# Performance work log

Measured on AMD Instinct MI355X. Metric: run time of the kernel, lower is better.

Reference implementation:

```python
import jax, jax.numpy as jnp
import numpy as np
import math

NUM_BUCKETS = 32
MAX_DISTANCE = 128
N_HEAD = 16
HEAD_DIM = 64
HIDDEN = 1024


def _rel_buckets(S):
    """T5 bidirectional relative-position buckets, [q, k] int32."""
    half = NUM_BUCKETS // 2            # 16
    max_exact = half // 2              # 8
    coeff = (half - max_exact) / math.log(MAX_DISTANCE / max_exact)
    pos = jnp.arange(S, dtype=jnp.int32)
    rel = pos[None, :] - pos[:, None]  # mem_pos - ctx_pos, shape [q, k]
    arel = jnp.abs(rel)
    base = jnp.where(rel > 0, half, 0)
    # log-spaced buckets for distant positions (trunc toward zero == floor here since arg >= 0)
    distant = max_exact + (
        jnp.log(jnp.maximum(arel, 1).astype(jnp.float32) / max_exact) * coeff
    ).astype(jnp.int32)
    distant = jnp.minimum(distant, half - 1)
    return base + jnp.where(arel < max_exact, arel, distant)


def setup_inputs() -> dict:
    key = jax.random.key(0)
    k1, k2, k3, k4 = jax.random.split(key, 4)
    B, S = 2, 2048
    std = 1.0 / math.sqrt(HIDDEN)
    x = jax.random.normal(k1, (B, S, HIDDEN), dtype=jnp.float32)
    emb_weight = jax.random.normal(k2, (NUM_BUCKETS, N_HEAD), dtype=jnp.float32) * 0.5
    qkv_w = jax.random.normal(k3, (3 * N_HEAD * HEAD_DIM, HIDDEN), dtype=jnp.float32) * std
    o_w = jax.random.normal(k4, (HIDDEN, N_HEAD * HEAD_DIM), dtype=jnp.float32) * std
    return {"x": x, "emb_weight": emb_weight, "qkv_w": qkv_w, "o_w": o_w}


def reference(x, emb_weight, qkv_w, o_w):
    B, S, D = x.shape
    qkv = x @ qkv_w.T                                   # [B, S, 3*H*hd]
    qkv = qkv.reshape(B, S, 3, N_HEAD, HEAD_DIM)
    q = qkv[:, :, 0].transpose(0, 2, 1, 3)              # [B, H, S, hd]
    k = qkv[:, :, 1].transpose(0, 2, 1, 3)
    v = qkv[:, :, 2].transpose(0, 2, 1, 3)
    bias = emb_weight[_rel_buckets(S)]                  # [q, k, H]
    bias = bias.transpose(2, 0, 1)[None]                # [1, H, q, k]
    scale = HEAD_DIM ** -0.5
    scores = jnp.einsum('bhqd,bhkd->bhqk', q, k) * scale + bias
    attn = jax.nn.softmax(scores, axis=-1)
    a = jnp.einsum('bhqk,bhkd->bhqd', attn, v)          # [B, H, S, hd]
    a = a.transpose(0, 2, 1, 3).reshape(B, S, N_HEAD * HEAD_DIM)
    return a @ o_w.T
```

## Files before the change

### kernel.cpp

```cpp
#include <hip/hip_runtime.h>

#define S_LEN 2048
#define NH 16
#define HD 64
#define DMODEL 1024

typedef __attribute__((ext_vector_type(8))) short bf16x8;
typedef __attribute__((ext_vector_type(4))) float f32x4;

__device__ inline unsigned short f2bf(float f) {
  union { float f; unsigned u; } v; v.f = f;
  unsigned r = v.u + 0x7FFFu + ((v.u >> 16) & 1u);
  return (unsigned short)(r >> 16);
}

__device__ inline void async16(void* lds, const void* g) {
  __builtin_amdgcn_global_load_lds((__attribute__((address_space(1))) void*)(g),
                                   (__attribute__((address_space(3))) void*)(lds),
                                   16, 0, 0);
}

__global__ __launch_bounds__(256) void prep_kernel(
    const float* __restrict__ x, const float* __restrict__ emb,
    const float* __restrict__ qkv_w, const float* __restrict__ o_w,
    unsigned short* __restrict__ xb, unsigned short* __restrict__ wb,
    unsigned short* __restrict__ ob, float* __restrict__ biasg) {
  if (blockIdx.x >= 8192) {
    int h = blockIdx.x - 8192;
    for (int i = threadIdx.x; i < 4095; i += 256) {
      int rel = i - 2047;
      int a = rel < 0 ? -rel : rel;
      int bucket;
      if (a < 8) bucket = a;
      else bucket = 8 + (a >= 12) + (a >= 16) + (a >= 23) + (a >= 32) +
                        (a >= 46) + (a >= 64) + (a >= 91);
      if (rel > 0) bucket += 16;
      biasg[h * 4096 + i] = emb[bucket * NH + h] * 1.4426950408889634f;
    }
    return;
  }
  const int NX = 2 * S_LEN * DMODEL / 4;
  const int NW = 3 * NH * HD * DMODEL / 4;
  int j = blockIdx.x * 256 + threadIdx.x;
  const float* s; unsigned short* d;
  if (j < NX)            { s = x;     d = xb; }
  else if (j < NX + NW)  { j -= NX;      s = qkv_w; d = wb; }
  else                   { j -= NX + NW; s = o_w;   d = ob; }
  float4 v = ((const float4*)s)[j];
  ushort4 p;
  p.x = f2bf(v.x); p.y = f2bf(v.y); p.z = f2bf(v.z); p.w = f2bf(v.w);
  ((ushort4*)d)[j] = p;
}

__global__ __launch_bounds__(256) void qkv_gemm_kernel(
    const unsigned short* __restrict__ xb, const unsigned short* __restrict__ wb,
    unsigned short* __restrict__ Qg, unsigned short* __restrict__ Kg,
    unsigned short* __restrict__ Vtg) {
  __shared__ __align__(16) char smem[32768];
  char* As = smem;
  char* Bs = smem + 16384;
  int bid = blockIdx.x;
  int swz = (bid & 7) * 96 + (bid >> 3);
  int bm = swz / 24, bn = swz % 24;
  const int tid = threadIdx.x, lane = tid & 63, wave = tid >> 6;
  const int wr = wave >> 1, wc = wave & 1, lg = lane >> 4, li = lane & 15;
  const char* Ag = (const char*)xb;
  const char* Bg = (const char*)wb;

  f32x4 acc[4][4];
#pragma unroll
  for (int i = 0; i < 4; ++i)
#pragma unroll
    for (int j = 0; j < 4; ++j) acc[i][j] = (f32x4){0.f, 0.f, 0.f, 0.f};

  auto stage = [&](int buf, int kt) {
#pragma unroll
    for (int r = 0; r < 2; ++r) {
      int c = wave * 2 + r;
      int linear = c * 1024 + lane * 16;
      int row = linear >> 6;
      int cb = (linear & 63) ^ ((row & 3) << 4);
      async16(As + buf * 8192 + c * 1024,
              Ag + (size_t)(bm * 128 + row) * 2048 + kt * 64 + cb);
      async16(Bs + buf * 8192 + c * 1024,
              Bg + (size_t)(bn * 128 + row) * 2048 + kt * 64 + cb);
    }
  };

  stage(0, 0);
  __syncthreads();
  for (int kt = 0; kt < 32; ++kt) {
    int cur = kt & 1;
    if (kt < 31) stage(cur ^ 1, kt + 1);
    const char* Ab = As + cur * 8192;
    const char* Bb = Bs + cur * 8192;
    bf16x8 af[4], bfr[4];
#pragma unroll
    for (int i = 0; i < 4; ++i) {
      int ra = wr * 64 + i * 16 + li;
      af[i] = *(const bf16x8*)(Ab + ra * 64 + ((lg * 16) ^ ((ra & 3) << 4)));
      int rb = wc * 64 + i * 16 + li;
      bfr[i] = *(const bf16x8*)(Bb + rb * 64 + ((lg * 16) ^ ((rb & 3) << 4)));
    }
#pragma unroll
    for (int i = 0; i < 4; ++i)
#pragma unroll
      for (int j = 0; j < 4; ++j)
        acc[i][j] = __builtin_amdgcn_mfma_f32_16x16x32_bf16(af[i], bfr[j], acc[i][j], 0, 0, 0);
    __syncthreads();
  }

  int n0 = bn * 128 + wc * 64;
  int which = n0 >> 10;
  int h = (n0 >> 6) & 15;
  if (which < 2) {
    unsigned short* dst = (which == 0) ? Qg : Kg;
    float scl = (which == 0) ? 0.18033688011112042f : 1.0f;
#pragma unroll
    for (int i = 0; i < 4; ++i)
#pragma unroll
      for (int j = 0; j < 4; ++j)
#pragma unroll
        for (int r = 0; r < 4; ++r) {
          int mr = bm * 128 + wr * 64 + i * 16 + lg * 4 + r;
          int b = mr >> 11, sIdx = mr & 2047;
          int d = j * 16 + li;
          dst[(((size_t)(b * NH + h)) * S_LEN + sIdx) * HD + d] = f2bf(acc[i][j][r] * scl);
        }
  } else {
    char* T = smem + wave * 8192;
#pragma unroll
    for (int i = 0; i < 4; ++i)
#pragma unroll
      for (int j = 0; j < 4; ++j)
#pragma unroll
        for (int r = 0; r < 4; ++r) {
          int sl = i * 16 + lg * 4 + r;
          int dd = j * 16 + li;
          *(unsigned short*)(T + dd * 128 + ((sl * 2) ^ ((dd & 7) << 4))) = f2bf(acc[i][j][r]);
        }
    int m0 = bm * 128 + wr * 64;
    int b = m0 >> 11, s0 = m0 & 2047;
#pragma unroll
    for (int r2 = 0; r2 < 8; ++r2) {
      int linear = r2 * 1024 + lane * 16;
      int dd = linear >> 7;
      int ts = linear & 127;
      bf16x8 v = *(const bf16x8*)(T + dd * 128 + (ts ^ ((dd & 7) << 4)));
      char* dstb = (char*)Vtg + (((size_t)(b * NH + h) * HD + dd) * S_LEN + s0) * 2 + ts;
      *(bf16x8*)dstb = v;
    }
  }
}

__global__ __launch_bounds__(256) void attn_kernel(
    const unsigned short* __restrict__ Qg, const unsigned short* __restrict__ Kg,
    const unsigned short* __restrict__ Vtg, const float* __restrict__ biasg,
    unsigned short* __restrict__ aout) {
  __shared__ __align__(16) char shbuf[16640];
  __shared__ float biasl[2112];

  int bid = blockIdx.x;
  int swz = (bid & 7) * 128 + (bid >> 3);
  int bh = swz >> 5;
  int qt = swz & 31;
  int b = bh >> 4, h = bh & 15;
  int qbase = qt * 64;
  const int tid = threadIdx.x, lane = tid & 63, wave = tid >> 6;
  const int lg = lane >> 4, li = lane & 15;
  const int qo = wave >> 1, kh = wave & 1;
  const int qsub = qo * 32;

  const char* Kbh = (const char*)Kg + (size_t)bh * S_LEN * HD * 2;
  const char* Vbh = (const char*)Vtg + (size_t)bh * HD * S_LEN * 2;
  const char* Qbh = (const char*)Qg + (size_t)bh * S_LEN * HD * 2;

  for (int i = tid; i < 2112; i += 256)
    biasl[i] = (i < 2111) ? biasg[h * 4096 + i + 1984 - qbase] : 0.f;

  bf16x8 qf[2][2];
#pragma unroll
  for (int m = 0; m < 2; ++m)
#pragma unroll
    for (int kk = 0; kk < 2; ++kk)
      qf[m][kk] = *(const bf16x8*)(Qbh + (size_t)(qbase + qsub + m * 16 + li) * 128 + kk * 64 + lg * 16);

  f32x4 Oa[2][4];
  float lrow[2][4];
#pragma unroll
  for (int m = 0; m < 2; ++m) {
#pragma unroll
    for (int dt = 0; dt < 4; ++dt) Oa[m][dt] = (f32x4){0.f, 0.f, 0.f, 0.f};
#pragma unroll
    for (int r = 0; r < 4; ++r) lrow[m][r] = 0.f;
  }
  char* Pw = shbuf + wave * 4096;

  __syncthreads();

  for (int t = 0; t < 16; ++t) {
    int kt = kh * 16 + t;

    f32x4 sc[2][4];
#pragma unroll
    for (int m = 0; m < 2; ++m)
#pragma unroll
      for (int nt = 0; nt < 4; ++nt) sc[m][nt] = (f32x4){0.f, 0.f, 0.f, 0.f};
#pragma unroll
    for (int kk = 0; kk < 2; ++kk) {
      bf16x8 kf[4];
#pragma unroll
      for (int nt = 0; nt < 4; ++nt)
        kf[nt] = *(const bf16x8*)(Kbh + (size_t)(kt * 64 + nt * 16 + li) * 128 + kk * 64 + lg * 16);
#pragma unroll
      for (int nt = 0; nt < 4; ++nt)
#pragma unroll
        for (int m = 0; m < 2; ++m)
          sc[m][nt] = __builtin_amdgcn_mfma_f32_16x16x32_bf16(qf[m][kk], kf[nt], sc[m][nt], 0, 0, 0);
    }

#pragma unroll
    for (int m = 0; m < 2; ++m) {
      int bb = kt * 64 + li + 63 - (qsub + m * 16 + lg * 4);
#pragma unroll
      for (int nt = 0; nt < 4; ++nt) {
#pragma unroll
        for (int r = 0; r < 4; ++r) {
          float p = exp2f(sc[m][nt][r] + biasl[bb + nt * 16 - r]);
          lrow[m][r] += p;
          unsigned u = __float_as_uint(p) + 0x8000u;
          int prow = m * 16 + lg * 4 + r;
          *(unsigned short*)(Pw + prow * 128 + ((nt * 32 + li * 2) ^ ((prow & 7) << 4))) =
              (unsigned short)(u >> 16);
        }
      }
    }
    __builtin_amdgcn_sched_barrier(0);

#pragma unroll
    for (int kk = 0; kk < 2; ++kk) {
      bf16x8 vf[4];
#pragma unroll
      for (int dt = 0; dt < 4; ++dt)
        vf[dt] = *(const bf16x8*)(Vbh + (size_t)(dt * 16 + li) * 4096 + kt * 128 + kk * 64 + lg * 16);
      bf16x8 pa[2];
#pragma unroll
      for (int m = 0; m < 2; ++m)
        pa[m] = *(const bf16x8*)(Pw + (m * 16 + li) * 128 + ((kk * 64 + lg * 16) ^ ((li & 7) << 4)));
#pragma unroll
      for (int dt = 0; dt < 4; ++dt)
#pragma unroll
        for (int m = 0; m < 2; ++m)
          Oa[m][dt] = __builtin_amdgcn_mfma_f32_16x16x32_bf16(pa[m], vf[dt], Oa[m][dt], 0, 0, 0);
    }
  }

  float lsum[2][4];
#pragma unroll
  for (int m = 0; m < 2; ++m)
#pragma unroll
    for (int r = 0; r < 4; ++r) {
      float tv = lrow[m][r];
#pragma unroll
      for (int off = 1; off < 16; off <<= 1)
        tv += __shfl_xor(tv, off, 64);
      lsum[m][r] = tv;
    }

  __syncthreads();
  float* mo = (float*)shbuf;
  float* lml = (float*)(shbuf + 16384);
  if (kh == 1) {
#pragma unroll
    for (int m = 0; m < 2; ++m)
#pragma unroll
      for (int dt = 0; dt < 4; ++dt)
#pragma unroll
        for (int r = 0; r < 4; ++r)
          mo[(qo * 32 + m * 16 + lg * 4 + r) * 64 + dt * 16 + li] = Oa[m][dt][r];
    if (li == 0)
#pragma unroll
      for (int m = 0; m < 2; ++m)
#pragma unroll
        for (int r = 0; r < 4; ++r)
          lml[qo * 32 + m * 16 + lg * 4 + r] = lsum[m][r];
  }
  __syncthreads();
  if (kh == 0) {
#pragma unroll
    for (int m = 0; m < 2; ++m) {
      float inv[4];
#pragma unroll
      for (int r = 0; r < 4; ++r)
        inv[r] = 1.0f / (lsum[m][r] + lml[qo * 32 + m * 16 + lg * 4 + r]);
#pragma unroll
      for (int dt = 0; dt < 4; ++dt)
#pragma unroll
        for (int r = 0; r < 4; ++r) {
          float o = Oa[m][dt][r] + mo[(qo * 32 + m * 16 + lg * 4 + r) * 64 + dt * 16 + li];
          int srow = qbase + qsub + m * 16 + lg * 4 + r;
          aout[((size_t)b * S_LEN + srow) * DMODEL + h * HD + dt * 16 + li] = f2bf(o * inv[r]);
        }
    }
  }
}

__global__ __launch_bounds__(256) void oproj_gemm_kernel(
    const unsigned short* __restrict__ ab, const unsigned short* __restrict__ ob,
    float* __restrict__ out) {
  __shared__ __align__(16) char smem[32768];
  char* As = smem;
  char* Bs = smem + 16384;
  int bid = blockIdx.x;
  int swz = (bid & 7) * 32 + (bid >> 3);
  int bm = swz >> 3, bn = swz & 7;
  const int tid = threadIdx.x, lane = tid & 63, wave = tid >> 6;
  const int wr = wave >> 1, wc = wave & 1, lg = lane >> 4, li = lane & 15;
  const char* Ag = (const char*)ab;
  const char* Bg = (const char*)ob;

  f32x4 acc[4][4];
#pragma unroll
  for (int i = 0; i < 4; ++i)
#pragma unroll
    for (int j = 0; j < 4; ++j) acc[i][j] = (f32x4){0.f, 0.f, 0.f, 0.f};

  auto stage = [&](int buf, int kt) {
#pragma unroll
    for (int r = 0; r < 2; ++r) {
      int c = wave * 2 + r;
      int linear = c * 1024 + lane * 16;
      int row = linear >> 6;
      int cb = (linear & 63) ^ ((row & 3) << 4);
      async16(As + buf * 8192 + c * 1024,
              Ag + (size_t)(bm * 128 + row) * 2048 + kt * 64 + cb);
      async16(Bs + buf * 8192 + c * 1024,
              Bg + (size_t)(bn * 128 + row) * 2048 + kt * 64 + cb);
    }
  };

  stage(0, 0);
  __syncthreads();
  for (int kt = 0; kt < 32; ++kt) {
    int cur = kt & 1;
    if (kt < 31) stage(cur ^ 1, kt + 1);
    const char* Ab = As + cur * 8192;
    const char* Bb = Bs + cur * 8192;
    bf16x8 af[4], bfr[4];
#pragma unroll
    for (int i = 0; i < 4; ++i) {
      int ra = wr * 64 + i * 16 + li;
      af[i] = *(const bf16x8*)(Ab + ra * 64 + ((lg * 16) ^ ((ra & 3) << 4)));
      int rb = wc * 64 + i * 16 + li;
      bfr[i] = *(const bf16x8*)(Bb + rb * 64 + ((lg * 16) ^ ((rb & 3) << 4)));
    }
#pragma unroll
    for (int i = 0; i < 4; ++i)
#pragma unroll
      for (int j = 0; j < 4; ++j)
        acc[i][j] = __builtin_amdgcn_mfma_f32_16x16x32_bf16(af[i], bfr[j], acc[i][j], 0, 0, 0);
    __syncthreads();
  }

#pragma unroll
  for (int i = 0; i < 4; ++i)
#pragma unroll
    for (int j = 0; j < 4; ++j)
#pragma unroll
      for (int r = 0; r < 4; ++r) {
        int mr = bm * 128 + wr * 64 + i * 16 + lg * 4 + r;
        int n = bn * 128 + wc * 64 + j * 16 + li;
        out[(size_t)mr * DMODEL + n] = acc[i][j][r];
      }
}

extern "C" void kernel_launch(void* const* d_in, const int* in_sizes, int n_in,
                              void* d_out, int out_size, void* d_ws, size_t ws_size,
                              hipStream_t stream) {
  const float* x     = (const float*)d_in[0];
  const float* emb   = (const float*)d_in[1];
  const float* qkv_w = (const float*)d_in[2];
  const float* o_w   = (const float*)d_in[3];
  char* ws = (char*)d_ws;
  unsigned short* xb = (unsigned short*)(ws);
  unsigned short* wb = (unsigned short*)(ws + 8388608);
  unsigned short* ob = (unsigned short*)(ws + 14680064);
  unsigned short* Qg = (unsigned short*)(ws + 16777216);
  unsigned short* Kg = (unsigned short*)(ws + 25165824);
  unsigned short* Vt = (unsigned short*)(ws + 33554432);
  unsigned short* ab = (unsigned short*)(ws + 41943040);
  float* biasg       = (float*)(ws + 50331648);
  float* out = (float*)d_out;

  prep_kernel<<<8208, 256, 0, stream>>>(x, emb, qkv_w, o_w, xb, wb, ob, biasg);
  qkv_gemm_kernel<<<768, 256, 0, stream>>>(xb, wb, Qg, Kg, Vt);
  attn_kernel<<<1024, 256, 0, stream>>>(Qg, Kg, Vt, biasg, ab);
  oproj_gemm_kernel<<<256, 256, 0, stream>>>(ab, ob, out);
}
```

Baseline: 259.7 us.

## Keep softmax P in registers by transposing QK^T MFMA operands

Swaps the A/B operands of the QK^T MFMA so each lane holds scores along the key dimension, letting the exponentiated probabilities be packed into bf16 pairs and fed directly as the A operand of the PV MFMA. This removes the per-wave LDS round-trip (scalar 16-bit stores, swizzle, vector reloads) and the sched barrier. V is loaded as split 8-byte halves to match the new k-ordering, and the row-sum reduction becomes a per-lane sum plus cross-group shuffles. The split V loads are narrower global accesses and the biasl indexing changes pattern, which could cost some memory efficiency.

New measurement: 312.9 us. +20.5%, slower.

```diff
diff --git a/kernel.cpp b/kernel.cpp
--- a/kernel.cpp
+++ b/kernel.cpp
@@ -7,6 +7,7 @@
 
 typedef __attribute__((ext_vector_type(8))) short bf16x8;
 typedef __attribute__((ext_vector_type(4))) float f32x4;
+typedef __attribute__((ext_vector_type(4))) unsigned int u32x4;
 
 __device__ inline unsigned short f2bf(float f) {
   union { float f; unsigned u; } v; v.f = f;
@@ -18,6 +19,12 @@
   __builtin_amdgcn_global_load_lds((__attribute__((address_space(1))) void*)(g),
                                    (__attribute__((address_space(3))) void*)(lds),
                                    16, 0, 0);
+}
+
+__device__ inline unsigned pkbf(float a, float b) {
+  unsigned ua = __float_as_uint(a) + 0x8000u;
+  unsigned ub = __float_as_uint(b) + 0x8000u;
+  return (ua >> 16) | (ub & 0xFFFF0000u);
 }
 
 __global__ __launch_bounds__(256) void prep_kernel(
@@ -186,20 +193,17 @@
       qf[m][kk] = *(const bf16x8*)(Qbh + (size_t)(qbase + qsub + m * 16 + li) * 128 + kk * 64 + lg * 16);
 
   f32x4 Oa[2][4];
-  float lrow[2][4];
-#pragma unroll
-  for (int m = 0; m < 2; ++m) {
+  float lsum[2] = {0.f, 0.f};
+#pragma unroll
+  for (int m = 0; m < 2; ++m)
 #pragma unroll
     for (int dt = 0; dt < 4; ++dt) Oa[m][dt] = (f32x4){0.f, 0.f, 0.f, 0.f};
-#pragma unroll
-    for (int r = 0; r < 4; ++r) lrow[m][r] = 0.f;
-  }
-  char* Pw = shbuf + wave * 4096;
 
   __syncthreads();
 
   for (int t = 0; t < 16; ++t) {
     int kt = kh * 16 + t;
+    const char* Kt = Kbh + (size_t)kt * 64 * 128;
 
     f32x4 sc[2][4];
 #pragma unroll
@@ -211,61 +215,71 @@
       bf16x8 kf[4];
 #pragma unroll
       for (int nt = 0; nt < 4; ++nt)
-        kf[nt] = *(const bf16x8*)(Kbh + (size_t)(kt * 64 + nt * 16 + li) * 128 + kk * 64 + lg * 16);
+        kf[nt] = *(const bf16x8*)(Kt + (nt * 16 + li) * 128 + kk * 64 + lg * 16);
 #pragma unroll
       for (int nt = 0; nt < 4; ++nt)
 #pragma unroll
         for (int m = 0; m < 2; ++m)
-          sc[m][nt] = __builtin_amdgcn_mfma_f32_16x16x32_bf16(qf[m][kk], kf[nt], sc[m][nt], 0, 0, 0);
-    }
-
+          sc[m][nt] = __builtin_amdgcn_mfma_f32_16x16x32_bf16(kf[nt], qf[m][kk], sc[m][nt], 0, 0, 0);
+    }
+
+    uint2 va[2][4], vb[2][4];
+#pragma unroll
+    for (int kk2 = 0; kk2 < 2; ++kk2)
+#pragma unroll
+      for (int dt = 0; dt < 4; ++dt) {
+        const char* vp = Vbh + (size_t)(dt * 16 + li) * 4096 + kt * 128 + kk2 * 64 + lg * 8;
+        va[kk2][dt] = *(const uint2*)vp;
+        vb[kk2][dt] = *(const uint2*)(vp + 32);
+      }
+
+    unsigned upk[2][4][2];
 #pragma unroll
     for (int m = 0; m < 2; ++m) {
-      int bb = kt * 64 + li + 63 - (qsub + m * 16 + lg * 4);
+      int bb = kt * 64 + lg * 4 + 63 - (qsub + m * 16) - li;
 #pragma unroll
       for (int nt = 0; nt < 4; ++nt) {
-#pragma unroll
-        for (int r = 0; r < 4; ++r) {
-          float p = exp2f(sc[m][nt][r] + biasl[bb + nt * 16 - r]);
-          lrow[m][r] += p;
-          unsigned u = __float_as_uint(p) + 0x8000u;
-          int prow = m * 16 + lg * 4 + r;
-          *(unsigned short*)(Pw + prow * 128 + ((nt * 32 + li * 2) ^ ((prow & 7) << 4))) =
-              (unsigned short)(u >> 16);
-        }
+        float p0 = exp2f(sc[m][nt][0] + biasl[bb + nt * 16 + 0]);
+        float p1 = exp2f(sc[m][nt][1] + biasl[bb + nt * 16 + 1]);
+        float p2 = exp2f(sc[m][nt][2] + biasl[bb + nt * 16 + 2]);
+        float p3 = exp2f(sc[m][nt][3] + biasl[bb + nt * 16 + 3]);
+        lsum[m] += (p0 + p1) + (p2 + p3);
+        upk[m][nt][0] = pkbf(p0, p1);
+        upk[m][nt][1] = pkbf(p2, p3);
       }
     }
-    __builtin_amdgcn_sched_barrier(0);
-
-#pragma unroll
-    for (int kk = 0; kk < 2; ++kk) {
-      bf16x8 vf[4];
-#pragma unroll
-      for (int dt = 0; dt < 4; ++dt)
-        vf[dt] = *(const bf16x8*)(Vbh + (size_t)(dt * 16 + li) * 4096 + kt * 128 + kk * 64 + lg * 16);
+
+#pragma unroll
+    for (int kk2 = 0; kk2 < 2; ++kk2) {
       bf16x8 pa[2];
 #pragma unroll
-      for (int m = 0; m < 2; ++m)
-        pa[m] = *(const bf16x8*)(Pw + (m * 16 + li) * 128 + ((kk * 64 + lg * 16) ^ ((li & 7) << 4)));
-#pragma unroll
-      for (int dt = 0; dt < 4; ++dt)
+      for (int m = 0; m < 2; ++m) {
+        u32x4 w = {upk[m][2 * kk2][0], upk[m][2 * kk2][1],
+                   upk[m][2 * kk2 + 1][0], upk[m][2 * kk2 + 1][1]};
+        pa[m] = __builtin_bit_cast(bf16x8, w);
+      }
+#pragma unroll
+      for (int dt = 0; dt < 4; ++dt) {
+        u32x4 w = {va[kk2][dt].x, va[kk2][dt].y, vb[kk2][dt].x, vb[kk2][dt].y};
+        bf16x8 vf = __builtin_bit_cast(bf16x8, w);
 #pragma unroll
         for (int m = 0; m < 2; ++m)
-          Oa[m][dt] = __builtin_amdgcn_mfma_f32_16x16x32_bf16(pa[m], vf[dt], Oa[m][dt], 0, 0, 0);
-    }
-  }
-
-  float lsum[2][4];
+          Oa[m][dt] = __builtin_amdgcn_mfma_f32_16x16x32_bf16(pa[m], vf, Oa[m][dt], 0, 0, 0);
+      }
+    }
+  }
+
+#pragma unroll
+  for (int m = 0; m < 2; ++m) {
+    lsum[m] += __shfl_xor(lsum[m], 16, 64);
+    lsum[m] += __shfl_xor(lsum[m], 32, 64);
+  }
+  float lq[2][4];
 #pragma unroll
   for (int m = 0; m < 2; ++m)
 #pragma unroll
-    for (int r = 0; r < 4; ++r) {
-      float tv = lrow[m][r];
-#pragma unroll
-      for (int off = 1; off < 16; off <<= 1)
-        tv += __shfl_xor(tv, off, 64);
-      lsum[m][r] = tv;
-    }
+    for (int r = 0; r < 4; ++r)
+      lq[m][r] = __shfl(lsum[m], lg * 4 + r, 64);
 
   __syncthreads();
   float* mo = (float*)shbuf;
@@ -283,7 +297,7 @@
       for (int m = 0; m < 2; ++m)
 #pragma unroll
         for (int r = 0; r < 4; ++r)
-          lml[qo * 32 + m * 16 + lg * 4 + r] = lsum[m][r];
+          lml[qo * 32 + m * 16 + lg * 4 + r] = lq[m][r];
   }
   __syncthreads();
   if (kh == 0) {
@@ -292,7 +306,7 @@
       float inv[4];
 #pragma unroll
       for (int r = 0; r < 4; ++r)
-        inv[r] = 1.0f / (lsum[m][r] + lml[qo * 32 + m * 16 + lg * 4 + r]);
+        inv[r] = 1.0f / (lq[m][r] + lml[qo * 32 + m * 16 + lg * 4 + r]);
 #pragma unroll
       for (int dt = 0; dt < 4; ++dt)
 #pragma unroll
```
